# Optimization experiments

Measured on AMD Instinct MI355X. Metric: run time of the kernel, lower is better.

Reference implementation:

```python
import jax, jax.numpy as jnp
import numpy as np

B, T, DH, DS, A = 32, 2048, 1024, 1024, 512

def setup_inputs() -> dict:
    key = jax.random.key(0)
    k1, k2, k3, k4, k5 = jax.random.split(key, 5)
    s = jax.random.normal(k1, (B, DS), dtype=jnp.float32)
    h = jax.random.normal(k2, (B, T, DH), dtype=jnp.float32)
    # glorot_uniform for W_a, U_a; uniform(-0.05, 0.05) for v_a (Keras defaults)
    lim_W = np.sqrt(6.0 / (DS + A)).astype(np.float32)
    lim_U = np.sqrt(6.0 / (DH + A)).astype(np.float32)
    W_a = jax.random.uniform(k3, (DS, A), minval=-lim_W, maxval=lim_W, dtype=jnp.float32)
    U_a = jax.random.uniform(k4, (DH, A), minval=-lim_U, maxval=lim_U, dtype=jnp.float32)
    v_a = jax.random.uniform(k5, (A,), minval=-0.05, maxval=0.05, dtype=jnp.float32)
    return {"s": s, "h": h, "W_a": W_a, "U_a": U_a, "v_a": v_a}

def reference(s, h, W_a, U_a, v_a):
    # U_a_h: [B, T, A]; W_a_s: [B, 1, A]
    U_a_h = jnp.einsum('btd,da->bta', h, U_a)
    W_a_s = (s @ W_a)[:, None, :]
    e = jnp.tanh(W_a_s + U_a_h)          # [B, T, A]
    e = jnp.einsum('bta,a->bt', e, v_a)   # learned-vector reduction
    a = jax.nn.softmax(e, axis=-1)        # exp / sum over time (same math, stable)
    c = jnp.einsum('bt,btd->bd', a, h)    # weighted sum over time
    return c
```

## Files before the change

### kernel.cpp

```cpp
#include <hip/hip_runtime.h>
#include <hip/hip_bf16.h>

#define B_  32
#define T_  2048
#define DH_ 1024
#define DS_ 1024
#define A_  512
#define M_  (B_ * T_)
#define NCH 16

typedef __attribute__((ext_vector_type(8))) short bf16x8;
typedef __attribute__((ext_vector_type(4))) float f32x4;

__device__ __forceinline__ unsigned short f2bf(float f) {
    union { float f; unsigned u; } v; v.f = f;
    unsigned r = 0x7FFFu + ((v.u >> 16) & 1u);
    return (unsigned short)((v.u + r) >> 16);
}
__device__ __forceinline__ float fast_tanh(float x) {
    float cx = fminf(fmaxf(x, -9.f), 9.f);
    float e2 = __expf(2.f * cx);
    return (e2 - 1.f) / (e2 + 1.f);
}
__device__ __forceinline__ unsigned pack_bf2(float lo, float hi) {
    union { float f; unsigned u; } a, b;
    a.f = lo; b.f = hi;
    return __builtin_amdgcn_perm(b.u + 0x8000u, a.u + 0x8000u, 0x07060302u);
}

__global__ void prep_ut(const float* __restrict__ U, unsigned short* __restrict__ Ut) {
    int o = blockIdx.x * 256 + threadIdx.x;
    int a = o >> 10, k = o & (DH_ - 1);
    Ut[o] = f2bf(U[k * A_ + a]);
}

__global__ void ws_gemv2(const float* __restrict__ s, const float* __restrict__ W,
                         float* __restrict__ Ws) {
    __shared__ float red[4][64];
    const int blk = blockIdx.x;
    const int b = blk >> 3, a0 = (blk & 7) * 64;
    const int tid = threadIdx.x;
    const int a = a0 + (tid & 63), kq = tid >> 6;
    const float* sp = s + b * DS_ + kq * 256;
    const float* wp = W + (size_t)(kq * 256) * A_ + a;
    float acc = 0.f;
#pragma unroll 8
    for (int k = 0; k < 256; ++k) acc += sp[k] * wp[(size_t)k * A_];
    red[kq][tid & 63] = acc;
    __syncthreads();
    if (tid < 64)
        Ws[b * A_ + a0 + tid] = red[0][tid] + red[1][tid] + red[2][tid] + red[3][tid];
}

__global__ void __launch_bounds__(512, 2)
fused_chunk(const float* __restrict__ h,
            const unsigned short* __restrict__ Ut,
            const float* __restrict__ Ws, const float* __restrict__ va,
            float* __restrict__ pm, float* __restrict__ pl,
            float* __restrict__ pc) {
    __shared__ unsigned short As[2][128][32];
    __shared__ unsigned short Bs[2][512][32];

    const int tid = threadIdx.x;
    const int tm = blockIdx.x;
    const int rowBase = tm * 128;

    const int lane = tid & 63;
    const int wid = tid >> 6;
    const int wm = wid >> 2, wn = wid & 3;
    const int lr = lane & 15, kg = lane >> 4;
    const int gsw16 = (kg ^ ((lr >> 1) & 3)) * 8;

    const int ar = tid >> 2;
    const int alg = tid & 3;

    f32x4 acc[4][8];
#pragma unroll
    for (int i = 0; i < 4; ++i)
#pragma unroll
        for (int j = 0; j < 8; ++j) acc[i][j] = (f32x4){0.f, 0.f, 0.f, 0.f};

    auto loadA = [&](float4* areg, int t) {
        const float* hp = h + (size_t)(rowBase + ar) * DH_ + t * 32 + alg * 8;
        areg[0] = *(const float4*)(hp);
        areg[1] = *(const float4*)(hp + 4);
    };
    auto stageB = [&](int buf, int t) {
        const int k0 = t * 32;
#pragma unroll
        for (int j = 0; j < 4; ++j) {
            int byt = j * 8192 + tid * 16;
            int r = byt >> 6;
            int g = ((byt >> 4) & 3) ^ ((r >> 1) & 3);
            const unsigned short* gb = Ut + (size_t)r * DH_ + k0 + g * 8;
            __builtin_amdgcn_global_load_lds(
                (const __attribute__((address_space(1))) unsigned int*)gb,
                (__attribute__((address_space(3))) unsigned int*)(&Bs[buf][0][0] + (byt >> 1)),
                16, 0, 0);
        }
    };
    auto packwriteA = [&](const float4* areg, int buf) {
        uint4 u;
        u.x = pack_bf2(areg[0].x, areg[0].y);
        u.y = pack_bf2(areg[0].z, areg[0].w);
        u.z = pack_bf2(areg[1].x, areg[1].y);
        u.w = pack_bf2(areg[1].z, areg[1].w);
        int p = alg ^ ((ar >> 1) & 3);
        *(uint4*)((char*)&As[buf][0][0] + ar * 64 + p * 16) = u;
    };

    float4 areg[2];
    const int NT = DH_ / 32;

    loadA(areg, 0);
    __builtin_amdgcn_sched_barrier(0);
    stageB(0, 0);
    __builtin_amdgcn_sched_barrier(0);
    packwriteA(areg, 0);
    asm volatile("s_waitcnt vmcnt(0) lgkmcnt(0)" ::: "memory");
    __builtin_amdgcn_s_barrier();
    __builtin_amdgcn_sched_barrier(0);

#pragma unroll 1
    for (int t = 0; t < NT; ++t) {
        const int buf = t & 1;
        const bool more = (t < NT - 1);
        if (more) {
            loadA(areg, t + 1);
            __builtin_amdgcn_sched_barrier(0);
            stageB(buf ^ 1, t + 1);
            __builtin_amdgcn_sched_barrier(0);
        }

        const unsigned short* Ab = &As[buf][0][0];
        const unsigned short* Bb = &Bs[buf][0][0];
        bf16x8 af[4], bq[8];
#pragma unroll
        for (int nf = 0; nf < 8; ++nf)
            bq[nf] = *(const bf16x8*)(Bb + (wn * 128 + nf * 16 + lr) * 32 + gsw16);
#pragma unroll
        for (int mi = 0; mi < 4; ++mi)
            af[mi] = *(const bf16x8*)(Ab + (wm * 64 + mi * 16 + lr) * 32 + gsw16);
        asm volatile("s_waitcnt lgkmcnt(0)" ::: "memory");
        __builtin_amdgcn_sched_barrier(0);

        __builtin_amdgcn_s_setprio(1);
#pragma unroll
        for (int mi = 0; mi < 4; ++mi)
#pragma unroll
            for (int nf = 0; nf < 8; ++nf)
                acc[mi][nf] = __builtin_amdgcn_mfma_f32_16x16x32_bf16(
                    af[mi], bq[nf], acc[mi][nf], 0, 0, 0);
        __builtin_amdgcn_s_setprio(0);
        __builtin_amdgcn_sched_barrier(0);

        if (more) {
            packwriteA(areg, buf ^ 1);
            asm volatile("s_waitcnt vmcnt(0) lgkmcnt(0)" ::: "memory");
            __builtin_amdgcn_s_barrier();
            __builtin_amdgcn_sched_barrier(0);
        }
    }
    __syncthreads();

    float* er_s  = (float*)&As[0][0][0];
    float* red_s = er_s + 128;
    float* w_s   = er_s + 256;
    float* pf    = er_s + 384;

    const int bIdx = rowBase >> 11;
    const float* WsRow = Ws + bIdx * A_;
    float wsv[8], vav[8];
#pragma unroll
    for (int nf = 0; nf < 8; ++nf) {
        int a = wn * 128 + nf * 16 + lr;
        wsv[nf] = WsRow[a];
        vav[nf] = va[a];
    }
#pragma unroll
    for (int mi = 0; mi < 4; ++mi) {
#pragma unroll
        for (int j = 0; j < 4; ++j) {
            float ssum = 0.f;
#pragma unroll
            for (int nf = 0; nf < 8; ++nf) {
                float x = acc[mi][nf][j] + wsv[nf];
                ssum += fast_tanh(x) * vav[nf];
            }
            ssum += __shfl_xor(ssum, 1);
            ssum += __shfl_xor(ssum, 2);
            ssum += __shfl_xor(ssum, 4);
            ssum += __shfl_xor(ssum, 8);
            if (lr == 0) {
                int r = wm * 64 + mi * 16 + kg * 4 + j;
                pf[r * 4 + wn] = ssum;
            }
        }
    }
    __syncthreads();
    if (tid < 128) {
        float v = pf[tid * 4] + pf[tid * 4 + 1] + pf[tid * 4 + 2] + pf[tid * 4 + 3];
        er_s[tid] = v;
        red_s[tid] = v;
    }
    __syncthreads();
    if (tid < 64) red_s[tid] = fmaxf(red_s[tid], red_s[tid + 64]);
    __syncthreads();
    if (tid < 32) red_s[tid] = fmaxf(red_s[tid], red_s[tid + 32]);
    __syncthreads();
    if (tid < 16) red_s[tid] = fmaxf(red_s[tid], red_s[tid + 16]);
    __syncthreads();
    if (tid < 8) red_s[tid] = fmaxf(red_s[tid], red_s[tid + 8]);
    __syncthreads();
    if (tid < 4) red_s[tid] = fmaxf(red_s[tid], red_s[tid + 4]);
    __syncthreads();
    if (tid < 2) red_s[tid] = fmaxf(red_s[tid], red_s[tid + 2]);
    __syncthreads();
    if (tid == 0) red_s[0] = fmaxf(red_s[0], red_s[1]);
    __syncthreads();
    const float mloc = red_s[0];
    __syncthreads();
    if (tid < 128) {
        float w = __expf(er_s[tid] - mloc);
        w_s[tid] = w;
        red_s[tid] = w;
    }
    __syncthreads();
    if (tid < 64) red_s[tid] += red_s[tid + 64];
    __syncthreads();
    if (tid < 32) red_s[tid] += red_s[tid + 32];
    __syncthreads();
    if (tid < 16) red_s[tid] += red_s[tid + 16];
    __syncthreads();
    if (tid < 8) red_s[tid] += red_s[tid + 8];
    __syncthreads();
    if (tid < 4) red_s[tid] += red_s[tid + 4];
    __syncthreads();
    if (tid < 2) red_s[tid] += red_s[tid + 2];
    __syncthreads();
    if (tid == 0) {
        pm[tm] = mloc;
        pl[tm] = red_s[0] + red_s[1];
    }

    float c0 = 0.f, c1 = 0.f;
    const float* hp = h + (size_t)rowBase * DH_ + tid;
#pragma unroll 4
    for (int t = 0; t < 128; ++t) {
        float w = w_s[t];
        c0 += w * hp[(size_t)t * DH_];
        c1 += w * hp[(size_t)t * DH_ + 512];
    }
    float* pcp = pc + (size_t)tm * DH_;
    pcp[tid] = c0;
    pcp[tid + 512] = c1;
}

__global__ void combine(const float* __restrict__ pm, const float* __restrict__ pl,
                        const float* __restrict__ pc, float* __restrict__ c) {
    const int b = blockIdx.x;
    const int tid = threadIdx.x;
    float M = -1e30f;
#pragma unroll
    for (int i = 0; i < NCH; ++i) M = fmaxf(M, pm[b * NCH + i]);
    float L = 0.f;
    float sc[NCH];
#pragma unroll
    for (int i = 0; i < NCH; ++i) {
        sc[i] = __expf(pm[b * NCH + i] - M);
        L += sc[i] * pl[b * NCH + i];
    }
    float a0 = 0.f, a1 = 0.f;
#pragma unroll
    for (int i = 0; i < NCH; ++i) {
        const float* pcp = pc + (size_t)(b * NCH + i) * DH_;
        a0 += sc[i] * pcp[tid];
        a1 += sc[i] * pcp[tid + 512];
    }
    const float inv = 1.f / L;
    c[(size_t)b * DH_ + tid] = a0 * inv;
    c[(size_t)b * DH_ + tid + 512] = a1 * inv;
}

extern "C" void kernel_launch(void* const* d_in, const int* in_sizes, int n_in,
                              void* d_out, int out_size, void* d_ws, size_t ws_size,
                              hipStream_t stream) {
    const float* s   = (const float*)d_in[0];
    const float* h   = (const float*)d_in[1];
    const float* W_a = (const float*)d_in[2];
    const float* U_a = (const float*)d_in[3];
    const float* v_a = (const float*)d_in[4];
    float* c = (float*)d_out;

    float* Ws = (float*)d_ws;
    unsigned short* Ut = (unsigned short*)(Ws + B_ * A_);
    float* pm = (float*)(Ut + (size_t)A_ * DH_);
    float* pl = pm + B_ * NCH;
    float* pc = pl + B_ * NCH;

    prep_ut<<<(A_ * DH_) / 256, 256, 0, stream>>>(U_a, Ut);
    ws_gemv2<<<B_ * 8, 256, 0, stream>>>(s, W_a, Ws);
    fused_chunk<<<B_ * NCH, 512, 0, stream>>>(h, Ut, Ws, v_a, pm, pl, pc);
    combine<<<B_, 512, 0, stream>>>(pm, pl, pc, c);
}
```

Before: 180.6 us.

## Split B tile into halves with a triple-buffered phase pipeline

Each K-step of the fused GEMM now runs as two phases, each covering half of the N columns (256 of 512). B-halves rotate through three LDS buffers, and the vmcnt waits are partial, so the next half's global-to-LDS load overlaps the current half's MFMAs. This hides load latency better than the earlier full-tile double buffer and lowers the LDS footprint. The cost is twice as many barriers per K-step, a remapped column layout in the epilogue, and delicate vmcnt accounting.

After: 198.8 us. 1.1x slower.

```diff
diff --git a/kernel.cpp b/kernel.cpp
--- a/kernel.cpp
+++ b/kernel.cpp
@@ -53,13 +53,13 @@
 }
 
 __global__ void __launch_bounds__(512, 2)
-fused_chunk(const float* __restrict__ h,
-            const unsigned short* __restrict__ Ut,
-            const float* __restrict__ Ws, const float* __restrict__ va,
-            float* __restrict__ pm, float* __restrict__ pl,
-            float* __restrict__ pc) {
+fused_ph(const float* __restrict__ h,
+         const unsigned short* __restrict__ Ut,
+         const float* __restrict__ Ws, const float* __restrict__ va,
+         float* __restrict__ pm, float* __restrict__ pl,
+         float* __restrict__ pc) {
     __shared__ unsigned short As[2][128][32];
-    __shared__ unsigned short Bs[2][512][32];
+    __shared__ unsigned short BsH[3][256][32];
 
     const int tid = threadIdx.x;
     const int tm = blockIdx.x;
@@ -85,17 +85,17 @@
         areg[0] = *(const float4*)(hp);
         areg[1] = *(const float4*)(hp + 4);
     };
-    auto stageB = [&](int buf, int t) {
+    auto stage_half = [&](int buf, int t, int p) {
         const int k0 = t * 32;
 #pragma unroll
-        for (int j = 0; j < 4; ++j) {
+        for (int j = 0; j < 2; ++j) {
             int byt = j * 8192 + tid * 16;
             int r = byt >> 6;
             int g = ((byt >> 4) & 3) ^ ((r >> 1) & 3);
-            const unsigned short* gb = Ut + (size_t)r * DH_ + k0 + g * 8;
+            const unsigned short* gb = Ut + (size_t)(p * 256 + r) * DH_ + k0 + g * 8;
             __builtin_amdgcn_global_load_lds(
                 (const __attribute__((address_space(1))) unsigned int*)gb,
-                (__attribute__((address_space(3))) unsigned int*)(&Bs[buf][0][0] + (byt >> 1)),
+                (__attribute__((address_space(3))) unsigned int*)(&BsH[buf][0][0] + (byt >> 1)),
                 16, 0, 0);
         }
     };
@@ -114,52 +114,108 @@
 
     loadA(areg, 0);
     __builtin_amdgcn_sched_barrier(0);
-    stageB(0, 0);
+    stage_half(0, 0, 0);
+    stage_half(1, 0, 1);
     __builtin_amdgcn_sched_barrier(0);
     packwriteA(areg, 0);
-    asm volatile("s_waitcnt vmcnt(0) lgkmcnt(0)" ::: "memory");
+    asm volatile("s_waitcnt vmcnt(2) lgkmcnt(0)" ::: "memory");
     __builtin_amdgcn_s_barrier();
     __builtin_amdgcn_sched_barrier(0);
 
 #pragma unroll 1
-    for (int t = 0; t < NT; ++t) {
-        const int buf = t & 1;
-        const bool more = (t < NT - 1);
-        if (more) {
-            loadA(areg, t + 1);
-            __builtin_amdgcn_sched_barrier(0);
-            stageB(buf ^ 1, t + 1);
-            __builtin_amdgcn_sched_barrier(0);
+    for (int t = 0; t < NT - 1; ++t) {
+        const int phi = 2 * t;
+        loadA(areg, t + 1);
+        __builtin_amdgcn_sched_barrier(0);
+        stage_half((phi + 2) % 3, t + 1, 0);
+        __builtin_amdgcn_sched_barrier(0);
+        bf16x8 af[4], bq[4];
+        {
+            const unsigned short* Ab = &As[t & 1][0][0];
+            const unsigned short* Bb = &BsH[phi % 3][0][0];
+#pragma unroll
+            for (int nfl = 0; nfl < 4; ++nfl)
+                bq[nfl] = *(const bf16x8*)(Bb + (wn * 64 + nfl * 16 + lr) * 32 + gsw16);
+#pragma unroll
+            for (int mi = 0; mi < 4; ++mi)
+                af[mi] = *(const bf16x8*)(Ab + (wm * 64 + mi * 16 + lr) * 32 + gsw16);
         }
-
-        const unsigned short* Ab = &As[buf][0][0];
-        const unsigned short* Bb = &Bs[buf][0][0];
-        bf16x8 af[4], bq[8];
-#pragma unroll
-        for (int nf = 0; nf < 8; ++nf)
-            bq[nf] = *(const bf16x8*)(Bb + (wn * 128 + nf * 16 + lr) * 32 + gsw16);
+        asm volatile("s_waitcnt lgkmcnt(0)" ::: "memory");
+        __builtin_amdgcn_sched_barrier(0);
+        __builtin_amdgcn_s_setprio(1);
+#pragma unroll
+        for (int mi = 0; mi < 4; ++mi)
+#pragma unroll
+            for (int nfl = 0; nfl < 4; ++nfl)
+                acc[mi][nfl] = __builtin_amdgcn_mfma_f32_16x16x32_bf16(
+                    af[mi], bq[nfl], acc[mi][nfl], 0, 0, 0);
+        __builtin_amdgcn_s_setprio(0);
+        __builtin_amdgcn_sched_barrier(0);
+        asm volatile("s_waitcnt vmcnt(10)" ::: "memory");
+        __builtin_amdgcn_s_barrier();
+        __builtin_amdgcn_sched_barrier(0);
+
+        stage_half((phi + 3) % 3, t + 1, 1);
+        __builtin_amdgcn_sched_barrier(0);
+        bf16x8 bq1[4];
+        {
+            const unsigned short* Bb = &BsH[(phi + 1) % 3][0][0];
+#pragma unroll
+            for (int nfl = 0; nfl < 4; ++nfl)
+                bq1[nfl] = *(const bf16x8*)(Bb + (wn * 64 + nfl * 16 + lr) * 32 + gsw16);
+        }
+        asm volatile("s_waitcnt lgkmcnt(0)" ::: "memory");
+        __builtin_amdgcn_sched_barrier(0);
+        __builtin_amdgcn_s_setprio(1);
+#pragma unroll
+        for (int mi = 0; mi < 4; ++mi)
+#pragma unroll
+            for (int nfl = 0; nfl < 4; ++nfl)
+                acc[mi][4 + nfl] = __builtin_amdgcn_mfma_f32_16x16x32_bf16(
+                    af[mi], bq1[nfl], acc[mi][4 + nfl], 0, 0, 0);
+        __builtin_amdgcn_s_setprio(0);
+        __builtin_amdgcn_sched_barrier(0);
+        packwriteA(areg, (t + 1) & 1);
+        asm volatile("s_waitcnt vmcnt(2) lgkmcnt(0)" ::: "memory");
+        __builtin_amdgcn_s_barrier();
+        __builtin_amdgcn_sched_barrier(0);
+    }
+
+    {
+        const int t = NT - 1, phi = 2 * t;
+        bf16x8 af[4], bq[4];
+        const unsigned short* Ab = &As[t & 1][0][0];
+        const unsigned short* Bb0 = &BsH[phi % 3][0][0];
+#pragma unroll
+        for (int nfl = 0; nfl < 4; ++nfl)
+            bq[nfl] = *(const bf16x8*)(Bb0 + (wn * 64 + nfl * 16 + lr) * 32 + gsw16);
 #pragma unroll
         for (int mi = 0; mi < 4; ++mi)
             af[mi] = *(const bf16x8*)(Ab + (wm * 64 + mi * 16 + lr) * 32 + gsw16);
         asm volatile("s_waitcnt lgkmcnt(0)" ::: "memory");
         __builtin_amdgcn_sched_barrier(0);
-
-        __builtin_amdgcn_s_setprio(1);
-#pragma unroll
-        for (int mi = 0; mi < 4; ++mi)
-#pragma unroll
-            for (int nf = 0; nf < 8; ++nf)
-                acc[mi][nf] = __builtin_amdgcn_mfma_f32_16x16x32_bf16(
-                    af[mi], bq[nf], acc[mi][nf], 0, 0, 0);
-        __builtin_amdgcn_s_setprio(0);
-        __builtin_amdgcn_sched_barrier(0);
-
-        if (more) {
-            packwriteA(areg, buf ^ 1);
-            asm volatile("s_waitcnt vmcnt(0) lgkmcnt(0)" ::: "memory");
-            __builtin_amdgcn_s_barrier();
-            __builtin_amdgcn_sched_barrier(0);
-        }
+#pragma unroll
+        for (int mi = 0; mi < 4; ++mi)
+#pragma unroll
+            for (int nfl = 0; nfl < 4; ++nfl)
+                acc[mi][nfl] = __builtin_amdgcn_mfma_f32_16x16x32_bf16(
+                    af[mi], bq[nfl], acc[mi][nfl], 0, 0, 0);
+        asm volatile("s_waitcnt vmcnt(0)" ::: "memory");
+        __builtin_amdgcn_s_barrier();
+        __builtin_amdgcn_sched_barrier(0);
+        const unsigned short* Bb1 = &BsH[(phi + 1) % 3][0][0];
+        bf16x8 bq1[4];
+#pragma unroll
+        for (int nfl = 0; nfl < 4; ++nfl)
+            bq1[nfl] = *(const bf16x8*)(Bb1 + (wn * 64 + nfl * 16 + lr) * 32 + gsw16);
+        asm volatile("s_waitcnt lgkmcnt(0)" ::: "memory");
+        __builtin_amdgcn_sched_barrier(0);
+#pragma unroll
+        for (int mi = 0; mi < 4; ++mi)
+#pragma unroll
+            for (int nfl = 0; nfl < 4; ++nfl)
+                acc[mi][4 + nfl] = __builtin_amdgcn_mfma_f32_16x16x32_bf16(
+                    af[mi], bq1[nfl], acc[mi][4 + nfl], 0, 0, 0);
     }
     __syncthreads();
 
@@ -173,7 +229,7 @@
     float wsv[8], vav[8];
 #pragma unroll
     for (int nf = 0; nf < 8; ++nf) {
-        int a = wn * 128 + nf * 16 + lr;
+        int a = (nf >> 2) * 256 + wn * 64 + (nf & 3) * 16 + lr;
         wsv[nf] = WsRow[a];
         vav[nf] = va[a];
     }
@@ -300,6 +356,6 @@
 
     prep_ut<<<(A_ * DH_) / 256, 256, 0, stream>>>(U_a, Ut);
     ws_gemv2<<<B_ * 8, 256, 0, stream>>>(s, W_a, Ws);
-    fused_chunk<<<B_ * NCH, 512, 0, stream>>>(h, Ut, Ws, v_a, pm, pl, pc);
+    fused_ph<<<B_ * NCH, 512, 0, stream>>>(h, Ut, Ws, v_a, pm, pl, pc);
     combine<<<B_, 512, 0, stream>>>(pm, pl, pc, c);
 }
```

## Load U_a fragments directly into registers and deepen A prefetch pipeline

Applied to the files above, without the earlier changes.

Drops the LDS staging buffer for the transposed U_a operand. Each wave now loads its B fragments straight from global memory into registers, double-buffered across k-steps, and the h tile is prefetched two steps ahead using two register sets. This removes LDS traffic and the vmcnt wait on B before each barrier, and frees 64KB of shared memory. In exchange, each wave redundantly reads B from global/L2 instead of sharing it through LDS, and register pressure rises under the 2-blocks-per-SM launch bound.

Measured after the change: 215.1 us. 19.1% more time.

```diff
diff --git a/kernel.cpp b/kernel.cpp
--- a/kernel.cpp
+++ b/kernel.cpp
@@ -53,13 +53,12 @@
 }
 
 __global__ void __launch_bounds__(512, 2)
-fused_chunk(const float* __restrict__ h,
-            const unsigned short* __restrict__ Ut,
-            const float* __restrict__ Ws, const float* __restrict__ va,
-            float* __restrict__ pm, float* __restrict__ pl,
-            float* __restrict__ pc) {
+fused_reg(const float* __restrict__ h,
+          const unsigned short* __restrict__ Ut,
+          const float* __restrict__ Ws, const float* __restrict__ va,
+          float* __restrict__ pm, float* __restrict__ pl,
+          float* __restrict__ pc) {
     __shared__ unsigned short As[2][128][32];
-    __shared__ unsigned short Bs[2][512][32];
 
     const int tid = threadIdx.x;
     const int tm = blockIdx.x;
@@ -85,19 +84,12 @@
         areg[0] = *(const float4*)(hp);
         areg[1] = *(const float4*)(hp + 4);
     };
-    auto stageB = [&](int buf, int t) {
-        const int k0 = t * 32;
-#pragma unroll
-        for (int j = 0; j < 4; ++j) {
-            int byt = j * 8192 + tid * 16;
-            int r = byt >> 6;
-            int g = ((byt >> 4) & 3) ^ ((r >> 1) & 3);
-            const unsigned short* gb = Ut + (size_t)r * DH_ + k0 + g * 8;
-            __builtin_amdgcn_global_load_lds(
-                (const __attribute__((address_space(1))) unsigned int*)gb,
-                (__attribute__((address_space(3))) unsigned int*)(&Bs[buf][0][0] + (byt >> 1)),
-                16, 0, 0);
-        }
+    const unsigned short* bbase = Ut + (size_t)(wn * 128 + lr) * DH_ + kg * 8;
+    auto loadB = [&](bf16x8* bq, int t) {
+        const unsigned short* bp = bbase + t * 32;
+#pragma unroll
+        for (int nf = 0; nf < 8; ++nf)
+            bq[nf] = *(const bf16x8*)(bp + (size_t)nf * 16 * DH_);
     };
     auto packwriteA = [&](const float4* areg, int buf) {
         uint4 u;
@@ -109,57 +101,84 @@
         *(uint4*)((char*)&As[buf][0][0] + ar * 64 + p * 16) = u;
     };
 
-    float4 areg[2];
+    float4 areg0[2], areg1[2];
+    bf16x8 bq0[8], bq1[8];
     const int NT = DH_ / 32;
 
-    loadA(areg, 0);
+    loadA(areg0, 0);
     __builtin_amdgcn_sched_barrier(0);
-    stageB(0, 0);
+    loadA(areg1, 1);
     __builtin_amdgcn_sched_barrier(0);
-    packwriteA(areg, 0);
-    asm volatile("s_waitcnt vmcnt(0) lgkmcnt(0)" ::: "memory");
+    loadB(bq0, 0);
+    __builtin_amdgcn_sched_barrier(0);
+    packwriteA(areg0, 0);
+    asm volatile("s_waitcnt lgkmcnt(0)" ::: "memory");
     __builtin_amdgcn_s_barrier();
     __builtin_amdgcn_sched_barrier(0);
 
+#define KSTEP(T_, BQ_C, BQ_N, AR_C, AR_N)                                     \
+    {                                                                         \
+        const int t_ = (T_);                                                  \
+        loadA(AR_N, t_ + 2);                                                  \
+        __builtin_amdgcn_sched_barrier(0);                                    \
+        loadB(BQ_N, t_ + 1);                                                  \
+        __builtin_amdgcn_sched_barrier(0);                                    \
+        bf16x8 af[4];                                                         \
+        const unsigned short* Ab = &As[t_ & 1][0][0];                         \
+        _Pragma("unroll")                                                     \
+        for (int mi = 0; mi < 4; ++mi)                                        \
+            af[mi] = *(const bf16x8*)(Ab + (wm * 64 + mi * 16 + lr) * 32 + gsw16); \
+        __builtin_amdgcn_s_setprio(1);                                        \
+        _Pragma("unroll")                                                     \
+        for (int mi = 0; mi < 4; ++mi)                                        \
+            _Pragma("unroll")                                                 \
+            for (int nf = 0; nf < 8; ++nf)                                    \
+                acc[mi][nf] = __builtin_amdgcn_mfma_f32_16x16x32_bf16(        \
+                    af[mi], BQ_C[nf], acc[mi][nf], 0, 0, 0);                  \
+        __builtin_amdgcn_s_setprio(0);                                        \
+        __builtin_amdgcn_sched_barrier(0);                                    \
+        packwriteA(AR_C, (t_ + 1) & 1);                                       \
+        asm volatile("s_waitcnt lgkmcnt(0)" ::: "memory");                    \
+        __builtin_amdgcn_s_barrier();                                         \
+        __builtin_amdgcn_sched_barrier(0);                                    \
+    }
+
 #pragma unroll 1
-    for (int t = 0; t < NT; ++t) {
-        const int buf = t & 1;
-        const bool more = (t < NT - 1);
-        if (more) {
-            loadA(areg, t + 1);
-            __builtin_amdgcn_sched_barrier(0);
-            stageB(buf ^ 1, t + 1);
-            __builtin_amdgcn_sched_barrier(0);
-        }
-
-        const unsigned short* Ab = &As[buf][0][0];
-        const unsigned short* Bb = &Bs[buf][0][0];
-        bf16x8 af[4], bq[8];
-#pragma unroll
-        for (int nf = 0; nf < 8; ++nf)
-            bq[nf] = *(const bf16x8*)(Bb + (wn * 128 + nf * 16 + lr) * 32 + gsw16);
+    for (int t = 0; t < NT - 2; t += 2) {
+        KSTEP(t, bq0, bq1, areg1, areg0);
+        KSTEP(t + 1, bq1, bq0, areg0, areg1);
+    }
+    {
+        loadB(bq1, NT - 1);
+        __builtin_amdgcn_sched_barrier(0);
+        bf16x8 af[4];
+        const unsigned short* Ab = &As[(NT - 2) & 1][0][0];
 #pragma unroll
         for (int mi = 0; mi < 4; ++mi)
             af[mi] = *(const bf16x8*)(Ab + (wm * 64 + mi * 16 + lr) * 32 + gsw16);
-        asm volatile("s_waitcnt lgkmcnt(0)" ::: "memory");
-        __builtin_amdgcn_sched_barrier(0);
-
-        __builtin_amdgcn_s_setprio(1);
 #pragma unroll
         for (int mi = 0; mi < 4; ++mi)
 #pragma unroll
             for (int nf = 0; nf < 8; ++nf)
                 acc[mi][nf] = __builtin_amdgcn_mfma_f32_16x16x32_bf16(
-                    af[mi], bq[nf], acc[mi][nf], 0, 0, 0);
-        __builtin_amdgcn_s_setprio(0);
+                    af[mi], bq0[nf], acc[mi][nf], 0, 0, 0);
+        packwriteA(areg1, (NT - 1) & 1);
+        asm volatile("s_waitcnt lgkmcnt(0)" ::: "memory");
+        __builtin_amdgcn_s_barrier();
         __builtin_amdgcn_sched_barrier(0);
-
-        if (more) {
-            packwriteA(areg, buf ^ 1);
-            asm volatile("s_waitcnt vmcnt(0) lgkmcnt(0)" ::: "memory");
-            __builtin_amdgcn_s_barrier();
-            __builtin_amdgcn_sched_barrier(0);
-        }
+    }
+    {
+        bf16x8 af[4];
+        const unsigned short* Ab = &As[(NT - 1) & 1][0][0];
+#pragma unroll
+        for (int mi = 0; mi < 4; ++mi)
+            af[mi] = *(const bf16x8*)(Ab + (wm * 64 + mi * 16 + lr) * 32 + gsw16);
+#pragma unroll
+        for (int mi = 0; mi < 4; ++mi)
+#pragma unroll
+            for (int nf = 0; nf < 8; ++nf)
+                acc[mi][nf] = __builtin_amdgcn_mfma_f32_16x16x32_bf16(
+                    af[mi], bq1[nf], acc[mi][nf], 0, 0, 0);
     }
     __syncthreads();
 
@@ -300,6 +319,6 @@
 
     prep_ut<<<(A_ * DH_) / 256, 256, 0, stream>>>(U_a, Ut);
     ws_gemv2<<<B_ * 8, 256, 0, stream>>>(s, W_a, Ws);
-    fused_chunk<<<B_ * NCH, 512, 0, stream>>>(h, Ut, Ws, v_a, pm, pl, pc);
+    fused_reg<<<B_ * NCH, 512, 0, stream>>>(h, Ut, Ws, v_a, pm, pl, pc);
     combine<<<B_, 512, 0, stream>>>(pm, pl, pc, c);
 }
```

## Split fused GEMM N dimension into two passes to halve accumulators and LDS

Applied to the files above, without the earlier changes.

The fused attention kernel now computes the 512-wide attention dimension in two passes of 256 columns. Each pass re-streams the h tile through the K loop and adds its tanh-weighted partial scores into a shared score buffer. This halves the accumulator registers and the B-tile LDS footprint, aiming for better occupancy or less spilling. The cost is reading h and converting it to bf16 twice per block, plus an extra pipeline prologue and extra barriers.

After: 227.7 us. +26.0%, slower.

```diff
diff --git a/kernel.cpp b/kernel.cpp
--- a/kernel.cpp
+++ b/kernel.cpp
@@ -53,13 +53,17 @@
 }
 
 __global__ void __launch_bounds__(512, 2)
-fused_chunk(const float* __restrict__ h,
-            const unsigned short* __restrict__ Ut,
-            const float* __restrict__ Ws, const float* __restrict__ va,
-            float* __restrict__ pm, float* __restrict__ pl,
-            float* __restrict__ pc) {
+fused_np2(const float* __restrict__ h,
+          const unsigned short* __restrict__ Ut,
+          const float* __restrict__ Ws, const float* __restrict__ va,
+          float* __restrict__ pm, float* __restrict__ pl,
+          float* __restrict__ pc) {
     __shared__ unsigned short As[2][128][32];
-    __shared__ unsigned short Bs[2][512][32];
+    __shared__ unsigned short Bs[2][256][32];
+    __shared__ float pf2[512];
+    __shared__ float er128[128];
+    __shared__ float red2[128];
+    __shared__ float w_s2[128];
 
     const int tid = threadIdx.x;
     const int tm = blockIdx.x;
@@ -74,25 +78,21 @@
     const int ar = tid >> 2;
     const int alg = tid & 3;
 
-    f32x4 acc[4][8];
-#pragma unroll
-    for (int i = 0; i < 4; ++i)
-#pragma unroll
-        for (int j = 0; j < 8; ++j) acc[i][j] = (f32x4){0.f, 0.f, 0.f, 0.f};
+    if (tid < 128) er128[tid] = 0.f;
 
     auto loadA = [&](float4* areg, int t) {
         const float* hp = h + (size_t)(rowBase + ar) * DH_ + t * 32 + alg * 8;
         areg[0] = *(const float4*)(hp);
         areg[1] = *(const float4*)(hp + 4);
     };
-    auto stageB = [&](int buf, int t) {
+    auto stageB = [&](int buf, int t, int nBase) {
         const int k0 = t * 32;
 #pragma unroll
-        for (int j = 0; j < 4; ++j) {
+        for (int j = 0; j < 2; ++j) {
             int byt = j * 8192 + tid * 16;
             int r = byt >> 6;
             int g = ((byt >> 4) & 3) ^ ((r >> 1) & 3);
-            const unsigned short* gb = Ut + (size_t)r * DH_ + k0 + g * 8;
+            const unsigned short* gb = Ut + (size_t)(nBase + r) * DH_ + k0 + g * 8;
             __builtin_amdgcn_global_load_lds(
                 (const __attribute__((address_space(1))) unsigned int*)gb,
                 (__attribute__((address_space(3))) unsigned int*)(&Bs[buf][0][0] + (byt >> 1)),
@@ -109,145 +109,152 @@
         *(uint4*)((char*)&As[buf][0][0] + ar * 64 + p * 16) = u;
     };
 
-    float4 areg[2];
     const int NT = DH_ / 32;
-
-    loadA(areg, 0);
-    __builtin_amdgcn_sched_barrier(0);
-    stageB(0, 0);
-    __builtin_amdgcn_sched_barrier(0);
-    packwriteA(areg, 0);
-    asm volatile("s_waitcnt vmcnt(0) lgkmcnt(0)" ::: "memory");
-    __builtin_amdgcn_s_barrier();
-    __builtin_amdgcn_sched_barrier(0);
-
-#pragma unroll 1
-    for (int t = 0; t < NT; ++t) {
-        const int buf = t & 1;
-        const bool more = (t < NT - 1);
-        if (more) {
-            loadA(areg, t + 1);
-            __builtin_amdgcn_sched_barrier(0);
-            stageB(buf ^ 1, t + 1);
-            __builtin_amdgcn_sched_barrier(0);
-        }
-
-        const unsigned short* Ab = &As[buf][0][0];
-        const unsigned short* Bb = &Bs[buf][0][0];
-        bf16x8 af[4], bq[8];
-#pragma unroll
-        for (int nf = 0; nf < 8; ++nf)
-            bq[nf] = *(const bf16x8*)(Bb + (wn * 128 + nf * 16 + lr) * 32 + gsw16);
-#pragma unroll
-        for (int mi = 0; mi < 4; ++mi)
-            af[mi] = *(const bf16x8*)(Ab + (wm * 64 + mi * 16 + lr) * 32 + gsw16);
-        asm volatile("s_waitcnt lgkmcnt(0)" ::: "memory");
-        __builtin_amdgcn_sched_barrier(0);
-
-        __builtin_amdgcn_s_setprio(1);
-#pragma unroll
-        for (int mi = 0; mi < 4; ++mi)
-#pragma unroll
-            for (int nf = 0; nf < 8; ++nf)
-                acc[mi][nf] = __builtin_amdgcn_mfma_f32_16x16x32_bf16(
-                    af[mi], bq[nf], acc[mi][nf], 0, 0, 0);
-        __builtin_amdgcn_s_setprio(0);
-        __builtin_amdgcn_sched_barrier(0);
-
-        if (more) {
-            packwriteA(areg, buf ^ 1);
-            asm volatile("s_waitcnt vmcnt(0) lgkmcnt(0)" ::: "memory");
-            __builtin_amdgcn_s_barrier();
-            __builtin_amdgcn_sched_barrier(0);
-        }
-    }
-    __syncthreads();
-
-    float* er_s  = (float*)&As[0][0][0];
-    float* red_s = er_s + 128;
-    float* w_s   = er_s + 256;
-    float* pf    = er_s + 384;
-
     const int bIdx = rowBase >> 11;
     const float* WsRow = Ws + bIdx * A_;
-    float wsv[8], vav[8];
-#pragma unroll
-    for (int nf = 0; nf < 8; ++nf) {
-        int a = wn * 128 + nf * 16 + lr;
-        wsv[nf] = WsRow[a];
-        vav[nf] = va[a];
-    }
-#pragma unroll
-    for (int mi = 0; mi < 4; ++mi) {
-#pragma unroll
-        for (int j = 0; j < 4; ++j) {
-            float ssum = 0.f;
-#pragma unroll
-            for (int nf = 0; nf < 8; ++nf) {
-                float x = acc[mi][nf][j] + wsv[nf];
-                ssum += fast_tanh(x) * vav[nf];
+
+#pragma unroll 1
+    for (int np = 0; np < 2; ++np) {
+        const int nBase = np * 256;
+
+        f32x4 acc[4][4];
+#pragma unroll
+        for (int i = 0; i < 4; ++i)
+#pragma unroll
+            for (int j = 0; j < 4; ++j) acc[i][j] = (f32x4){0.f, 0.f, 0.f, 0.f};
+
+        float4 areg[2];
+        loadA(areg, 0);
+        __builtin_amdgcn_sched_barrier(0);
+        stageB(0, 0, nBase);
+        __builtin_amdgcn_sched_barrier(0);
+        packwriteA(areg, 0);
+        asm volatile("s_waitcnt vmcnt(0) lgkmcnt(0)" ::: "memory");
+        __builtin_amdgcn_s_barrier();
+        __builtin_amdgcn_sched_barrier(0);
+
+#pragma unroll 1
+        for (int t = 0; t < NT; ++t) {
+            const int buf = t & 1;
+            const bool more = (t < NT - 1);
+            if (more) {
+                loadA(areg, t + 1);
+                __builtin_amdgcn_sched_barrier(0);
+                stageB(buf ^ 1, t + 1, nBase);
+                __builtin_amdgcn_sched_barrier(0);
             }
-            ssum += __shfl_xor(ssum, 1);
-            ssum += __shfl_xor(ssum, 2);
-            ssum += __shfl_xor(ssum, 4);
-            ssum += __shfl_xor(ssum, 8);
-            if (lr == 0) {
-                int r = wm * 64 + mi * 16 + kg * 4 + j;
-                pf[r * 4 + wn] = ssum;
+
+            const unsigned short* Ab = &As[buf][0][0];
+            const unsigned short* Bb = &Bs[buf][0][0];
+            bf16x8 af[4], bq[4];
+#pragma unroll
+            for (int nf = 0; nf < 4; ++nf)
+                bq[nf] = *(const bf16x8*)(Bb + (wn * 64 + nf * 16 + lr) * 32 + gsw16);
+#pragma unroll
+            for (int mi = 0; mi < 4; ++mi)
+                af[mi] = *(const bf16x8*)(Ab + (wm * 64 + mi * 16 + lr) * 32 + gsw16);
+            asm volatile("s_waitcnt lgkmcnt(0)" ::: "memory");
+            __builtin_amdgcn_sched_barrier(0);
+
+            __builtin_amdgcn_s_setprio(1);
+#pragma unroll
+            for (int mi = 0; mi < 4; ++mi)
+#pragma unroll
+                for (int nf = 0; nf < 4; ++nf)
+                    acc[mi][nf] = __builtin_amdgcn_mfma_f32_16x16x32_bf16(
+                        af[mi], bq[nf], acc[mi][nf], 0, 0, 0);
+            __builtin_amdgcn_s_setprio(0);
+            __builtin_amdgcn_sched_barrier(0);
+
+            if (more) {
+                packwriteA(areg, buf ^ 1);
+                asm volatile("s_waitcnt vmcnt(0) lgkmcnt(0)" ::: "memory");
+                __builtin_amdgcn_s_barrier();
+                __builtin_amdgcn_sched_barrier(0);
             }
         }
-    }
+        __syncthreads();
+
+        float wsv[4], vav[4];
+#pragma unroll
+        for (int nf = 0; nf < 4; ++nf) {
+            int a = nBase + wn * 64 + nf * 16 + lr;
+            wsv[nf] = WsRow[a];
+            vav[nf] = va[a];
+        }
+#pragma unroll
+        for (int mi = 0; mi < 4; ++mi) {
+#pragma unroll
+            for (int j = 0; j < 4; ++j) {
+                float ssum = 0.f;
+#pragma unroll
+                for (int nf = 0; nf < 4; ++nf) {
+                    float x = acc[mi][nf][j] + wsv[nf];
+                    ssum += fast_tanh(x) * vav[nf];
+                }
+                ssum += __shfl_xor(ssum, 1);
+                ssum += __shfl_xor(ssum, 2);
+                ssum += __shfl_xor(ssum, 4);
+                ssum += __shfl_xor(ssum, 8);
+                if (lr == 0) {
+                    int r = wm * 64 + mi * 16 + kg * 4 + j;
+                    pf2[r * 4 + wn] = ssum;
+                }
+            }
+        }
+        __syncthreads();
+        if (tid < 128)
+            er128[tid] += pf2[tid * 4] + pf2[tid * 4 + 1]
+                        + pf2[tid * 4 + 2] + pf2[tid * 4 + 3];
+        __syncthreads();
+    }
+
+    if (tid < 128) red2[tid] = er128[tid];
+    __syncthreads();
+    if (tid < 64) red2[tid] = fmaxf(red2[tid], red2[tid + 64]);
+    __syncthreads();
+    if (tid < 32) red2[tid] = fmaxf(red2[tid], red2[tid + 32]);
+    __syncthreads();
+    if (tid < 16) red2[tid] = fmaxf(red2[tid], red2[tid + 16]);
+    __syncthreads();
+    if (tid < 8) red2[tid] = fmaxf(red2[tid], red2[tid + 8]);
+    __syncthreads();
+    if (tid < 4) red2[tid] = fmaxf(red2[tid], red2[tid + 4]);
+    __syncthreads();
+    if (tid < 2) red2[tid] = fmaxf(red2[tid], red2[tid + 2]);
+    __syncthreads();
+    if (tid == 0) red2[0] = fmaxf(red2[0], red2[1]);
+    __syncthreads();
+    const float mloc = red2[0];
     __syncthreads();
     if (tid < 128) {
-        float v = pf[tid * 4] + pf[tid * 4 + 1] + pf[tid * 4 + 2] + pf[tid * 4 + 3];
-        er_s[tid] = v;
-        red_s[tid] = v;
-    }
-    __syncthreads();
-    if (tid < 64) red_s[tid] = fmaxf(red_s[tid], red_s[tid + 64]);
-    __syncthreads();
-    if (tid < 32) red_s[tid] = fmaxf(red_s[tid], red_s[tid + 32]);
-    __syncthreads();
-    if (tid < 16) red_s[tid] = fmaxf(red_s[tid], red_s[tid + 16]);
-    __syncthreads();
-    if (tid < 8) red_s[tid] = fmaxf(red_s[tid], red_s[tid + 8]);
-    __syncthreads();
-    if (tid < 4) red_s[tid] = fmaxf(red_s[tid], red_s[tid + 4]);
-    __syncthreads();
-    if (tid < 2) red_s[tid] = fmaxf(red_s[tid], red_s[tid + 2]);
-    __syncthreads();
-    if (tid == 0) red_s[0] = fmaxf(red_s[0], red_s[1]);
-    __syncthreads();
-    const float mloc = red_s[0];
-    __syncthreads();
-    if (tid < 128) {
-        float w = __expf(er_s[tid] - mloc);
-        w_s[tid] = w;
-        red_s[tid] = w;
-    }
-    __syncthreads();
-    if (tid < 64) red_s[tid] += red_s[tid + 64];
-    __syncthreads();
-    if (tid < 32) red_s[tid] += red_s[tid + 32];
-    __syncthreads();
-    if (tid < 16) red_s[tid] += red_s[tid + 16];
-    __syncthreads();
-    if (tid < 8) red_s[tid] += red_s[tid + 8];
-    __syncthreads();
-    if (tid < 4) red_s[tid] += red_s[tid + 4];
-    __syncthreads();
-    if (tid < 2) red_s[tid] += red_s[tid + 2];
+        float w = __expf(er128[tid] - mloc);
+        w_s2[tid] = w;
+        red2[tid] = w;
+    }
+    __syncthreads();
+    if (tid < 64) red2[tid] += red2[tid + 64];
+    __syncthreads();
+    if (tid < 32) red2[tid] += red2[tid + 32];
+    __syncthreads();
+    if (tid < 16) red2[tid] += red2[tid + 16];
+    __syncthreads();
+    if (tid < 8) red2[tid] += red2[tid + 8];
+    __syncthreads();
+    if (tid < 4) red2[tid] += red2[tid + 4];
+    __syncthreads();
+    if (tid < 2) red2[tid] += red2[tid + 2];
     __syncthreads();
     if (tid == 0) {
         pm[tm] = mloc;
-        pl[tm] = red_s[0] + red_s[1];
+        pl[tm] = red2[0] + red2[1];
     }
 
     float c0 = 0.f, c1 = 0.f;
     const float* hp = h + (size_t)rowBase * DH_ + tid;
 #pragma unroll 4
     for (int t = 0; t < 128; ++t) {
-        float w = w_s[t];
+        float w = w_s2[t];
         c0 += w * hp[(size_t)t * DH_];
         c1 += w * hp[(size_t)t * DH_ + 512];
     }
@@ -300,6 +307,6 @@
 
     prep_ut<<<(A_ * DH_) / 256, 256, 0, stream>>>(U_a, Ut);
     ws_gemv2<<<B_ * 8, 256, 0, stream>>>(s, W_a, Ws);
-    fused_chunk<<<B_ * NCH, 512, 0, stream>>>(h, Ut, Ws, v_a, pm, pl, pc);
+    fused_np2<<<B_ * NCH, 512, 0, stream>>>(h, Ut, Ws, v_a, pm, pl, pc);
     combine<<<B_, 512, 0, stream>>>(pm, pl, pc, c);
 }
```
